# Performance work log

Hardware: AMD Instinct MI355X
Metric: run time of the kernel (lower is better)

## Reference

```python
import jax, jax.numpy as jnp
import numpy as np

N_NODES = 100000
N_EDGES = 3200000
F_IN = 16
HID = 64
K = 4
N_LAYERS = 3
SLOPE = 0.01  # LeakyReLU default negative slope


def _gcn_norm(src, dst, edge_weight, n):
    # PyG gcn_norm with add_self_loops=False: deg over targets
    deg = jax.ops.segment_sum(edge_weight, dst, num_segments=n)
    dinv = jnp.where(deg > 0, jax.lax.rsqrt(jnp.maximum(deg, 1e-30)), 0.0)
    return dinv[src] * edge_weight * dinv[dst]


def _tag_conv(x, src, dst, norm, Ws, b):
    # out = sum_{k=0..K} (A_norm^k x) @ Ws[k] + b ; Ws: [K+1, in, out]
    out = x @ Ws[0]
    h = x
    for k in range(1, Ws.shape[0]):
        msg = norm[:, None] * h[src]                      # [E, in]
        h = jax.ops.segment_sum(msg, dst, num_segments=x.shape[0])
        out = out + h @ Ws[k]
    return out + b


def leaky_relu(x):
    return jnp.where(x >= 0, x, SLOPE * x)


def setup_inputs() -> dict:
    key = jax.random.key(0)
    ks = jax.random.split(key, 10)
    x = jax.random.normal(ks[0], (N_NODES, F_IN), dtype=jnp.float32)
    edge_index = jax.random.randint(ks[1], (2, N_EDGES), 0, N_NODES, dtype=jnp.int64)
    edge_weight = jax.random.uniform(ks[2], (N_EDGES,), dtype=jnp.float32)
    batch = jnp.zeros((N_NODES,), dtype=jnp.int64)
    s1 = 1.0 / np.sqrt(F_IN)
    s2 = 1.0 / np.sqrt(HID)
    W1 = jax.random.uniform(ks[3], (K + 1, F_IN, HID), jnp.float32, -s1, s1)
    b1 = jnp.zeros((HID,), jnp.float32)
    W2 = jax.random.uniform(ks[4], (N_LAYERS - 1, K + 1, HID, HID), jnp.float32, -s2, s2)
    b2 = jnp.zeros((N_LAYERS - 1, HID), jnp.float32)
    Wout = jax.random.uniform(ks[5], (HID, 1), jnp.float32, -s2, s2)
    bout = jnp.zeros((1,), jnp.float32)
    return {"x": x, "edge_index": edge_index, "edge_weight": edge_weight,
            "batch": batch, "W1": W1, "b1": b1, "W2": W2, "b2": b2,
            "Wout": Wout, "bout": bout}


def reference(x, edge_index, edge_weight, batch, W1, b1, W2, b2, Wout, bout):
    src, dst = edge_index[0], edge_index[1]
    norm = _gcn_norm(src, dst, edge_weight, x.shape[0])
    h = _tag_conv(x, src, dst, norm, W1, b1)
    h = leaky_relu(h)  # dropout p=0 -> identity (inference)
    for i in range(N_LAYERS - 1):
        h = _tag_conv(h, src, dst, norm, W2[i], b2[i])
        h = leaky_relu(h)
    # reghead_layers == 1 -> singleLinear
    return h @ Wout + bout
```

## Files before the change

### kernel.cpp

```cpp
#include <hip/hip_runtime.h>


typedef unsigned long long u64;
typedef unsigned int u32;

__device__ __forceinline__ float h2f(unsigned short u) {
  _Float16 h;
  __builtin_memcpy(&h, &u, 2);
  return (float)h;
}
__device__ __forceinline__ unsigned short f2h(float f) {
  _Float16 h = (_Float16)f;
  unsigned short u;
  __builtin_memcpy(&u, &h, 2);
  return u;
}
__device__ __forceinline__ ushort4 pack_h(float4 v) {
  ushort4 r;
  r.x = f2h(v.x); r.y = f2h(v.y); r.z = f2h(v.z); r.w = f2h(v.w);
  return r;
}
__device__ __forceinline__ float4 unpack_h(ushort4 u) {
  return make_float4(h2f(u.x), h2f(u.y), h2f(u.z), h2f(u.w));
}

__device__ __forceinline__ void fmix_lo(float& acc, u32 wsh, u32 h) {
  asm("v_fma_mix_f32 %0, %1, %2, %0 op_sel:[1,0,0] op_sel_hi:[1,1,0]"
      : "+v"(acc) : "v"(wsh), "v"(h));
}
__device__ __forceinline__ void fmix_hi(float& acc, u32 wsh, u32 h) {
  asm("v_fma_mix_f32 %0, %1, %2, %0 op_sel:[1,1,0] op_sel_hi:[1,1,0]"
      : "+v"(acc) : "v"(wsh), "v"(h));
}


__global__ __launch_bounds__(256) void k_hist(const int* __restrict__ dst, u32* __restrict__ H,
                                              int E, int CH, int NB,
                                              const float4* __restrict__ x4,
                                              ushort4* __restrict__ xh, int n4) {
  __shared__ u32 hc[1024];
  int tid = threadIdx.x, blk = blockIdx.x, nblk = gridDim.x;
  for (int i = tid; i < 1024; i += 256) hc[i] = 0;
  for (int i = blk * 256 + tid; i < n4; i += nblk * 256) xh[i] = pack_h(x4[i]);
  __syncthreads();
  int e0 = blk * CH, e1 = min(E, e0 + CH);
  for (int e = e0 + tid; e < e1; e += 256) atomicAdd(&hc[((u32)dst[e]) >> 7], 1u);
  __syncthreads();
  for (int c = tid; c < NB; c += 256) H[(size_t)c * nblk + blk] = hc[c];
}

__global__ void scanH_blocks(u32* __restrict__ H, u32* __restrict__ bsum, int n) {
  __shared__ u32 s[256];
  int tid = threadIdx.x;
  int i = blockIdx.x * 256 + tid;
  u32 v = (i < n) ? H[i] : 0;
  s[tid] = v;
  __syncthreads();
#pragma unroll
  for (int off = 1; off < 256; off <<= 1) {
    u32 t = (tid >= off) ? s[tid - off] : 0;
    __syncthreads();
    s[tid] += t;
    __syncthreads();
  }
  if (i < n) H[i] = s[tid] - v;
  if (tid == 255) bsum[blockIdx.x] = s[255];
}

__global__ void scanH_sums(u32* __restrict__ bsum, int nb) {
  __shared__ u32 s[1024];
  __shared__ u32 carry;
  int tid = threadIdx.x;
  if (tid == 0) carry = 0;
  __syncthreads();
  for (int base = 0; base < nb; base += 1024) {
    int i = base + tid;
    u32 v = (i < nb) ? bsum[i] : 0;
    s[tid] = v;
    __syncthreads();
#pragma unroll
    for (int off = 1; off < 1024; off <<= 1) {
      u32 t = (tid >= off) ? s[tid - off] : 0;
      __syncthreads();
      s[tid] += t;
      __syncthreads();
    }
    u32 c = carry;
    if (i < nb) bsum[i] = s[tid] - v + c;
    __syncthreads();
    if (tid == 1023) carry = c + s[1023];
    __syncthreads();
  }
}

__global__ void scanH_add(u32* __restrict__ H, const u32* __restrict__ bsum, int n) {
  int i = blockIdx.x * blockDim.x + threadIdx.x;
  if (i < n) H[i] += bsum[i >> 8];
}

__global__ __launch_bounds__(256) void k_scatter(const int* __restrict__ src,
                                                 const int* __restrict__ dst,
                                                 const float* __restrict__ w,
                                                 const u32* __restrict__ H,
                                                 u64* __restrict__ sorted, int E, int CH, int NB) {
  __shared__ u32 cur[1024];
  int tid = threadIdx.x, blk = blockIdx.x, nblk = gridDim.x;
  for (int c = tid; c < NB; c += 256) cur[c] = H[(size_t)c * nblk + blk];
  __syncthreads();
  int e0 = blk * CH, e1 = min(E, e0 + CH);
  for (int e = e0 + tid; e < e1; e += 256) {
    int d = dst[e];
    int c = ((u32)d) >> 7;
    u32 p = atomicAdd(&cur[c], 1u);
    u64 it = (u64)(u32)src[e] | ((u64)((u32)d & 127u) << 17) |
             ((u64)__float_as_uint(w[e]) << 24);
    sorted[p] = it;
  }
}

#define BCAP 6144
__global__ __launch_bounds__(256) void k_bucket(u64* __restrict__ sorted,
                                                const u32* __restrict__ H, int NBLK,
                                                int* __restrict__ ptr, float* __restrict__ dinv,
                                                int N, int E, int NB) {
  __shared__ u64 stage[BCAP];
  __shared__ u32 cnt[128], base[128], cur[128], tmp[128];
  __shared__ float ws[128];
  int c = blockIdx.x, tid = threadIdx.x;
  int b0 = (int)H[(size_t)c * NBLK];
  int b1 = (c + 1 < NB) ? (int)H[(size_t)(c + 1) * NBLK] : E;
  int m = b1 - b0;
  if (tid < 128) { cnt[tid] = 0; ws[tid] = 0.f; }
  __syncthreads();
  for (int i = tid; i < m; i += 256) {
    u64 it = sorted[b0 + i];
    stage[i] = it;
    int lo = (int)((it >> 17) & 127u);
    atomicAdd(&cnt[lo], 1u);
    atomicAdd(&ws[lo], __uint_as_float((u32)(it >> 24)));
  }
  __syncthreads();
  u32 v = (tid < 128) ? cnt[tid] : 0;
  if (tid < 128) tmp[tid] = v;
  __syncthreads();
#pragma unroll
  for (int off = 1; off < 128; off <<= 1) {
    u32 t = 0;
    if (tid < 128 && tid >= off) t = tmp[tid - off];
    __syncthreads();
    if (tid < 128) tmp[tid] += t;
    __syncthreads();
  }
  if (tid < 128) {
    base[tid] = tmp[tid] - v;
    cur[tid] = tmp[tid] - v;
    int node = c * 128 + tid;
    if (node < N) {
      ptr[node] = b0 + (int)base[tid];
      float d = ws[tid];
      dinv[node] = (d > 0.f) ? rsqrtf(fmaxf(d, 1e-30f)) : 0.f;
    }
  }
  if (c == NB - 1 && tid == 0) ptr[N] = E;
  __syncthreads();
  for (int i = tid; i < m; i += 256) {
    u64 it = stage[i];
    int lo = (int)((it >> 17) & 127u);
    u32 p = atomicAdd(&cur[lo], 1u);
    sorted[b0 + (int)p] = it;
  }
}

__global__ __launch_bounds__(256) void k_pack(const u64* __restrict__ sorted,
                                              const float* __restrict__ dinv,
                                              const u32* __restrict__ H, int NBLK,
                                              u32* __restrict__ ep, int E, int NB) {
  int c = blockIdx.x;
  int b0 = (int)H[(size_t)c * NBLK];
  int b1 = (c + 1 < NB) ? (int)H[(size_t)(c + 1) * NBLK] : E;
  for (int i = b0 + threadIdx.x; i < b1; i += 256) {
    u64 it = sorted[i];
    int s = (int)(it & 0x1FFFFu);
    int dn = c * 128 + (int)((it >> 17) & 127u);
    float wv = __uint_as_float((u32)(it >> 24));
    float nv = dinv[s] * wv * dinv[dn];
    ep[i] = ((u32)f2h(nv) << 17) | (u32)s;
  }
}

__device__ __forceinline__ void acc_e2(float4& a, u32 pe, uint2 hh) {
  u32 wsh = pe >> 1;
  fmix_lo(a.x, wsh, hh.x); fmix_hi(a.y, wsh, hh.x);
  fmix_lo(a.z, wsh, hh.y); fmix_hi(a.w, wsh, hh.y);
}

template <int F4>
__device__ __forceinline__ float4 gather(const int* __restrict__ ptr, const u32* __restrict__ ep,
                                         const ushort4* __restrict__ hin, int node, int f4) {
  int e0 = ptr[node], e1 = ptr[node + 1];
  float4 a = make_float4(0.f, 0.f, 0.f, 0.f);
  int e = e0;
  while (e < e1 && (e & 3)) {
    u32 pe = ep[e];
    acc_e2(a, pe, *(const uint2*)(hin + ((u32)(pe & 0x1FFFFu) * F4 + f4)));
    ++e;
  }
  int nq = (e1 - e) >> 2;
  if (nq > 0) {
    uint4 p = *(const uint4*)(ep + e);
    uint2 h0 = *(const uint2*)(hin + ((u32)(p.x & 0x1FFFFu) * F4 + f4));
    uint2 h1 = *(const uint2*)(hin + ((u32)(p.y & 0x1FFFFu) * F4 + f4));
    uint2 h2 = *(const uint2*)(hin + ((u32)(p.z & 0x1FFFFu) * F4 + f4));
    uint2 h3 = *(const uint2*)(hin + ((u32)(p.w & 0x1FFFFu) * F4 + f4));
    for (int q = 1; q < nq; ++q) {
      uint4 pn = *(const uint4*)(ep + e + 4 * q);
      uint2 g0 = *(const uint2*)(hin + ((u32)(pn.x & 0x1FFFFu) * F4 + f4));
      uint2 g1 = *(const uint2*)(hin + ((u32)(pn.y & 0x1FFFFu) * F4 + f4));
      uint2 g2 = *(const uint2*)(hin + ((u32)(pn.z & 0x1FFFFu) * F4 + f4));
      uint2 g3 = *(const uint2*)(hin + ((u32)(pn.w & 0x1FFFFu) * F4 + f4));
      acc_e2(a, p.x, h0); acc_e2(a, p.y, h1);
      acc_e2(a, p.z, h2); acc_e2(a, p.w, h3);
      p = pn; h0 = g0; h1 = g1; h2 = g2; h3 = g3;
    }
    acc_e2(a, p.x, h0); acc_e2(a, p.y, h1);
    acc_e2(a, p.z, h2); acc_e2(a, p.w, h3);
    e += nq * 4;
  }
  while (e < e1) {
    u32 pe = ep[e];
    acc_e2(a, pe, *(const uint2*)(hin + ((u32)(pe & 0x1FFFFu) * F4 + f4)));
    ++e;
  }
  return a;
}

__device__ __forceinline__ void acc8(float4& a0, float4& a1, u32 pe, uint4 r) {
  u32 wsh = pe >> 1;
  fmix_lo(a0.x, wsh, r.x); fmix_hi(a0.y, wsh, r.x);
  fmix_lo(a0.z, wsh, r.y); fmix_hi(a0.w, wsh, r.y);
  fmix_lo(a1.x, wsh, r.z); fmix_hi(a1.y, wsh, r.z);
  fmix_lo(a1.z, wsh, r.w); fmix_hi(a1.w, wsh, r.w);
}

__device__ __forceinline__ uint4 row16(const ushort4* __restrict__ hin, u32 pe, u32 foff) {
  return *(const uint4*)(hin + ((u32)(pe & 0x1FFFFu) * 16u + foff));
}

__device__ __forceinline__ void gather64o(const int* __restrict__ ptr, const u32* __restrict__ ep,
                                          const ushort4* __restrict__ hin, int node,
                                          int f8, int o, float4& a0, float4& a1) {
  int e0 = ptr[node], e1 = ptr[node + 1];
  const u32 foff = 2u * (u32)f8;
  int e = e0;
  while (e < e1 && (e & 3)) {
    if ((e & 1) == o) {
      u32 pe = ep[e];
      acc8(a0, a1, pe, row16(hin, pe, foff));
    }
    ++e;
  }
  int nq = (e1 - e) >> 2;
  int m = (nq > o) ? ((nq - o + 1) >> 1) : 0;
  const u32* qb = ep + e + 4 * o;
  if (m > 0) {
    uint4 pA = *(const uint4*)(qb);
    uint4 A0 = row16(hin, pA.x, foff), A1 = row16(hin, pA.y, foff);
    uint4 A2 = row16(hin, pA.z, foff), A3 = row16(hin, pA.w, foff);
    int j = 0;
    while (j + 2 < m) {
      uint4 pB = *(const uint4*)(qb + 8 * (j + 1));
      uint4 B0 = row16(hin, pB.x, foff), B1 = row16(hin, pB.y, foff);
      uint4 B2 = row16(hin, pB.z, foff), B3 = row16(hin, pB.w, foff);
      acc8(a0, a1, pA.x, A0); acc8(a0, a1, pA.y, A1);
      acc8(a0, a1, pA.z, A2); acc8(a0, a1, pA.w, A3);
      pA = *(const uint4*)(qb + 8 * (j + 2));
      A0 = row16(hin, pA.x, foff); A1 = row16(hin, pA.y, foff);
      A2 = row16(hin, pA.z, foff); A3 = row16(hin, pA.w, foff);
      acc8(a0, a1, pB.x, B0); acc8(a0, a1, pB.y, B1);
      acc8(a0, a1, pB.z, B2); acc8(a0, a1, pB.w, B3);
      j += 2;
    }
    if (j + 1 < m) {
      uint4 pB = *(const uint4*)(qb + 8 * (j + 1));
      uint4 B0 = row16(hin, pB.x, foff), B1 = row16(hin, pB.y, foff);
      uint4 B2 = row16(hin, pB.z, foff), B3 = row16(hin, pB.w, foff);
      acc8(a0, a1, pA.x, A0); acc8(a0, a1, pA.y, A1);
      acc8(a0, a1, pA.z, A2); acc8(a0, a1, pA.w, A3);
      acc8(a0, a1, pB.x, B0); acc8(a0, a1, pB.y, B1);
      acc8(a0, a1, pB.z, B2); acc8(a0, a1, pB.w, B3);
    } else {
      acc8(a0, a1, pA.x, A0); acc8(a0, a1, pA.y, A1);
      acc8(a0, a1, pA.z, A2); acc8(a0, a1, pA.w, A3);
    }
  }
  e += nq * 4;
  while (e < e1) {
    if ((e & 1) == o) {
      u32 pe = ep[e];
      acc8(a0, a1, pe, row16(hin, pe, foff));
    }
    ++e;
  }
}

__device__ __forceinline__ void mm_acc(const float* __restrict__ tl, const float4* __restrict__ Wl,
                                       int ln, int j4, float4& a) {
#pragma unroll 8
  for (int i = 0; i < 64; ++i) {
    float tv = tl[ln * 64 + ((((i >> 2) ^ ln) << 2) | (i & 3))];
    float4 wv = Wl[i * 16 + j4];
    a.x = fmaf(tv, wv.x, a.x); a.y = fmaf(tv, wv.y, a.y);
    a.z = fmaf(tv, wv.z, a.z); a.w = fmaf(tv, wv.w, a.w);
  }
}

template <bool FIRST, bool LAST, bool HEAD>
__launch_bounds__(256, 8)
__global__ void ptag64_k(const int* __restrict__ ptr, const u32* __restrict__ ep,
                         const ushort4* __restrict__ hin, ushort4* __restrict__ hout,
                         const float4* __restrict__ Wk4, const float4* __restrict__ W04,
                         ushort4* __restrict__ acch, const float4* __restrict__ bias4,
                         const float* __restrict__ Wout, const float* __restrict__ bout,
                         float* __restrict__ outv, int n) {
  __shared__ float4 Wl[1024];
  __shared__ float4 tl4[256];
  const float* tl = (const float*)tl4;
  int tid = threadIdx.x;
  for (int i = tid; i < 1024; i += 256) Wl[i] = Wk4[i];
  int gid = blockIdx.x * 256 + tid;
  int node = gid >> 4, j4 = gid & 15, ln = tid >> 4;
  const int o = j4 >> 3, f8 = j4 & 7;

  float4 a0 = make_float4(0.f, 0.f, 0.f, 0.f);
  float4 a1 = make_float4(0.f, 0.f, 0.f, 0.f);
  if (node < n) gather64o(ptr, ep, hin, node, f8, o, a0, a1);
  a0.x += __shfl_xor(a0.x, 8, 16); a0.y += __shfl_xor(a0.y, 8, 16);
  a0.z += __shfl_xor(a0.z, 8, 16); a0.w += __shfl_xor(a0.w, 8, 16);
  a1.x += __shfl_xor(a1.x, 8, 16); a1.y += __shfl_xor(a1.y, 8, 16);
  a1.z += __shfl_xor(a1.z, 8, 16); a1.w += __shfl_xor(a1.w, 8, 16);
  float4 t = (o == 0) ? a0 : a1;
  int g = 2 * f8 + o;
  if (node < n && !LAST) hout[(size_t)node * 16 + g] = pack_h(t);
  tl4[ln * 16 + (g ^ ln)] = t;
  __syncthreads();

  float4 a = make_float4(0.f, 0.f, 0.f, 0.f);
  if (!FIRST && node < n) a = unpack_h(acch[(size_t)node * 16 + j4]);
  mm_acc(tl, Wl, ln, j4, a);
  if (FIRST) {
    __syncthreads();
    for (int i = tid; i < 1024; i += 256) Wl[i] = W04[i];
    float4 own = make_float4(0.f, 0.f, 0.f, 0.f);
    if (node < n) own = unpack_h(hin[(size_t)node * 16 + j4]);
    tl4[ln * 16 + (j4 ^ ln)] = own;
    __syncthreads();
    mm_acc(tl, Wl, ln, j4, a);
  }
  if (node >= n) return;

  if (LAST) {
    float4 b = bias4[j4];
    a.x += b.x; a.y += b.y; a.z += b.z; a.w += b.w;
    a.x = (a.x >= 0.f) ? a.x : 0.01f * a.x;
    a.y = (a.y >= 0.f) ? a.y : 0.01f * a.y;
    a.z = (a.z >= 0.f) ? a.z : 0.01f * a.z;
    a.w = (a.w >= 0.f) ? a.w : 0.01f * a.w;
    if (HEAD) {
      float v = a.x * Wout[4 * j4] + a.y * Wout[4 * j4 + 1] +
                a.z * Wout[4 * j4 + 2] + a.w * Wout[4 * j4 + 3];
      v += __shfl_down(v, 8, 16);
      v += __shfl_down(v, 4, 16);
      v += __shfl_down(v, 2, 16);
      v += __shfl_down(v, 1, 16);
      if (j4 == 0) outv[node] = v + bout[0];
    } else {
      hout[(size_t)node * 16 + j4] = pack_h(a);
    }
  } else {
    acch[(size_t)node * 16 + j4] = pack_h(a);
  }
}

template <bool FIRST, bool LAST>
__launch_bounds__(256)
__global__ void ptag16_k(const int* __restrict__ ptr, const u32* __restrict__ ep,
                         const ushort4* __restrict__ hin, ushort4* __restrict__ hout,
                         const float4* __restrict__ Wk4, const float4* __restrict__ W04,
                         ushort4* __restrict__ acch, const float4* __restrict__ bias4,
                         ushort4* __restrict__ outbuf, int n) {
  __shared__ float4 Wl[256];
  __shared__ float4 W0l[FIRST ? 256 : 1];
  __shared__ float4 tl4[64 * 5];
  const float* tl = (const float*)tl4;
  int tid = threadIdx.x;
  Wl[tid] = Wk4[tid];
  if (FIRST) W0l[tid] = W04[tid];
  int gid = blockIdx.x * 256 + tid;
  int node = gid >> 2, q = tid & 3, ln = tid >> 2;

  float4 t = make_float4(0.f, 0.f, 0.f, 0.f);
  if (node < n) {
    t = gather<4>(ptr, ep, hin, node, q);
    if (!LAST) hout[(size_t)node * 4 + q] = pack_h(t);
  }
  tl4[ln * 5 + q] = t;
  __syncthreads();

  float4 a[4];
#pragma unroll
  for (int c = 0; c < 4; ++c) a[c] = make_float4(0.f, 0.f, 0.f, 0.f);
  if (!FIRST && node < n) {
#pragma unroll
    for (int c = 0; c < 4; ++c) a[c] = unpack_h(acch[(size_t)node * 16 + 4 * q + c]);
  }
#pragma unroll 4
  for (int i = 0; i < 16; ++i) {
    float tv = tl[ln * 20 + i];
#pragma unroll
    for (int c = 0; c < 4; ++c) {
      float4 wv = Wl[i * 16 + 4 * q + c];
      a[c].x = fmaf(tv, wv.x, a[c].x); a[c].y = fmaf(tv, wv.y, a[c].y);
      a[c].z = fmaf(tv, wv.z, a[c].z); a[c].w = fmaf(tv, wv.w, a[c].w);
    }
  }
  if (FIRST) {
    __syncthreads();
    float4 own = make_float4(0.f, 0.f, 0.f, 0.f);
    if (node < n) own = unpack_h(hin[(size_t)node * 4 + q]);
    tl4[ln * 5 + q] = own;
    __syncthreads();
#pragma unroll 4
    for (int i = 0; i < 16; ++i) {
      float tv = tl[ln * 20 + i];
#pragma unroll
      for (int c = 0; c < 4; ++c) {
        float4 wv = W0l[i * 16 + 4 * q + c];
        a[c].x = fmaf(tv, wv.x, a[c].x); a[c].y = fmaf(tv, wv.y, a[c].y);
        a[c].z = fmaf(tv, wv.z, a[c].z); a[c].w = fmaf(tv, wv.w, a[c].w);
      }
    }
  }
  if (node >= n) return;

  if (LAST) {
#pragma unroll
    for (int c = 0; c < 4; ++c) {
      float4 b = bias4[4 * q + c];
      a[c].x += b.x; a[c].y += b.y; a[c].z += b.z; a[c].w += b.w;
      a[c].x = (a[c].x >= 0.f) ? a[c].x : 0.01f * a[c].x;
      a[c].y = (a[c].y >= 0.f) ? a[c].y : 0.01f * a[c].y;
      a[c].z = (a[c].z >= 0.f) ? a[c].z : 0.01f * a[c].z;
      a[c].w = (a[c].w >= 0.f) ? a[c].w : 0.01f * a[c].w;
      outbuf[(size_t)node * 16 + 4 * q + c] = pack_h(a[c]);
    }
  } else {
#pragma unroll
    for (int c = 0; c < 4; ++c) acch[(size_t)node * 16 + 4 * q + c] = pack_h(a[c]);
  }
}

extern "C" void kernel_launch(void* const* d_in, const int* in_sizes, int n_in,
                              void* d_out, int out_size, void* d_ws, size_t ws_size,
                              hipStream_t stream) {
  const float* x    = (const float*)d_in[0];
  const int*   ei   = (const int*)d_in[1];
  const float* ew   = (const float*)d_in[2];
  const float* W1   = (const float*)d_in[4];
  const float* b1   = (const float*)d_in[5];
  const float* W2   = (const float*)d_in[6];
  const float* b2   = (const float*)d_in[7];
  const float* Wout = (const float*)d_in[8];
  const float* bout = (const float*)d_in[9];
  float* out = (float*)d_out;

  const int N = in_sizes[0] / 16;
  const int E = in_sizes[2];
  const int* src = ei;
  const int* dst = ei + E;

  const int NBH = 1024;
  const int CH = (E + NBH - 1) / NBH;
  const int NB = (N + 127) >> 7;
  const int HN = NB * NBH;

  char* ws = (char*)d_ws;
  size_t off = 0;
  auto alloc = [&](size_t bytes) {
    char* p = ws + off;
    off = (off + bytes + 255) & ~(size_t)255;
    return p;
  };
  u32*     H      = (u32*)alloc((size_t)HN * 4);
  u32*     bsum   = (u32*)alloc(16384);
  float*   dinv   = (float*)alloc((size_t)N * 4);
  int*     ptr    = (int*)alloc(((size_t)N + 1) * 4);
  u64*     sorted = (u64*)alloc((size_t)E * 8);
  u32*     ep     = (u32*)alloc((size_t)E * 4);
  ushort4* xh     = (ushort4*)alloc((size_t)N * 16 * 2);
  ushort4* hb0    = (ushort4*)alloc((size_t)N * 64 * 2);
  ushort4* hb1    = (ushort4*)alloc((size_t)N * 64 * 2);
  ushort4* hb2    = (ushort4*)alloc((size_t)N * 64 * 2);
  ushort4* acch   = (ushort4*)alloc((size_t)N * 64 * 2);

  k_hist<<<NBH, 256, 0, stream>>>(dst, H, E, CH, NB, (const float4*)x, xh, N * 4);
  scanH_blocks<<<HN / 256, 256, 0, stream>>>(H, bsum, HN);
  scanH_sums<<<1, 1024, 0, stream>>>(bsum, HN / 256);
  scanH_add<<<HN / 256, 256, 0, stream>>>(H, bsum, HN);
  k_scatter<<<NBH, 256, 0, stream>>>(src, dst, ew, H, sorted, E, CH, NB);
  k_bucket<<<NB, 256, 0, stream>>>(sorted, H, NBH, ptr, dinv, N, E, NB);
  k_pack<<<NB, 256, 0, stream>>>(sorted, dinv, H, NBH, ep, E, NB);

  int g4  = (N * 4 + 255) / 256;
  int g16 = (N * 16 + 255) / 256;

  auto W1k = [&](int k) { return (const float4*)(W1 + (size_t)k * 1024); };
  auto W2k = [&](int l, int k) { return (const float4*)(W2 + ((size_t)l * 5 + k) * 4096); };

  ptag16_k<true,  false><<<g4, 256, 0, stream>>>(ptr, ep, xh,  hb0, W1k(1), W1k(0), acch, nullptr, nullptr, N);
  ptag16_k<false, false><<<g4, 256, 0, stream>>>(ptr, ep, hb0, hb1, W1k(2), nullptr, acch, nullptr, nullptr, N);
  ptag16_k<false, false><<<g4, 256, 0, stream>>>(ptr, ep, hb1, hb0, W1k(3), nullptr, acch, nullptr, nullptr, N);
  ptag16_k<false, true ><<<g4, 256, 0, stream>>>(ptr, ep, hb0, nullptr, W1k(4), nullptr, acch,
                                                 (const float4*)b1, hb2, N);

  ptag64_k<true,  false, false><<<g16, 256, 0, stream>>>(ptr, ep, hb2, hb0, W2k(0,1), W2k(0,0), acch,
                                                         nullptr, nullptr, nullptr, nullptr, N);
  ptag64_k<false, false, false><<<g16, 256, 0, stream>>>(ptr, ep, hb0, hb1, W2k(0,2), nullptr, acch,
                                                         nullptr, nullptr, nullptr, nullptr, N);
  ptag64_k<false, false, false><<<g16, 256, 0, stream>>>(ptr, ep, hb1, hb0, W2k(0,3), nullptr, acch,
                                                         nullptr, nullptr, nullptr, nullptr, N);
  ptag64_k<false, true,  false><<<g16, 256, 0, stream>>>(ptr, ep, hb0, hb2, W2k(0,4), nullptr, acch,
                                                         (const float4*)b2, nullptr, nullptr, nullptr, N);
  ptag64_k<true,  false, false><<<g16, 256, 0, stream>>>(ptr, ep, hb2, hb0, W2k(1,1), W2k(1,0), acch,
                                                         nullptr, nullptr, nullptr, nullptr, N);
  ptag64_k<false, false, false><<<g16, 256, 0, stream>>>(ptr, ep, hb0, hb1, W2k(1,2), nullptr, acch,
                                                         nullptr, nullptr, nullptr, nullptr, N);
  ptag64_k<false, false, false><<<g16, 256, 0, stream>>>(ptr, ep, hb1, hb0, W2k(1,3), nullptr, acch,
                                                         nullptr, nullptr, nullptr, nullptr, N);
  ptag64_k<false, true,  true ><<<g16, 256, 0, stream>>>(ptr, ep, hb0, nullptr, W2k(1,4), nullptr, acch,
                                                         (const float4*)(b2 + 64), Wout, bout, out, N);
}
```

Before: 922.0 us.

## Locally sort edges per block in LDS before coalesced scatter to buckets

The scatter kernel now processes two histogram chunks per block. It builds a local bucket histogram and prefix scan in shared memory, then computes a local permutation of edge indices. Writes to the global sorted array then go out in bucket-contiguous runs, giving more coalesced stores than random per-edge scattered writes. The cost is an extra pass over dst, more shared memory (which can lower occupancy), and reliance on the chunk fitting SIDX_CAP and on the H offsets of consecutive blocks being contiguous per bucket.

```diff
diff --git a/kernel.cpp b/kernel.cpp
--- a/kernel.cpp
+++ b/kernel.cpp
@@ -98,23 +98,55 @@
   if (i < n) H[i] += bsum[i >> 8];
 }
 
-__global__ __launch_bounds__(256) void k_scatter(const int* __restrict__ src,
-                                                 const int* __restrict__ dst,
-                                                 const float* __restrict__ w,
-                                                 const u32* __restrict__ H,
-                                                 u64* __restrict__ sorted, int E, int CH, int NB) {
-  __shared__ u32 cur[1024];
-  int tid = threadIdx.x, blk = blockIdx.x, nblk = gridDim.x;
-  for (int c = tid; c < NB; c += 256) cur[c] = H[(size_t)c * nblk + blk];
-  __syncthreads();
-  int e0 = blk * CH, e1 = min(E, e0 + CH);
+#define SIDX_CAP 6400
+__global__ __launch_bounds__(256) void k_scatter2(const int* __restrict__ src,
+                                                  const int* __restrict__ dst,
+                                                  const float* __restrict__ w,
+                                                  const u32* __restrict__ H,
+                                                  u64* __restrict__ sorted,
+                                                  int E, int CH, int NB, int NBHIST) {
+  __shared__ u32 cnt[1024], base[1024], cur[1024], Hb[1024];
+  __shared__ u32 tmp[256];
+  __shared__ unsigned short sidx[SIDX_CAP];
+  int tid = threadIdx.x, blk = blockIdx.x;
+  int e0 = blk * 2 * CH, e1 = min(E, e0 + 2 * CH);
+  int m = e1 - e0;
+  for (int c = tid; c < 1024; c += 256) cnt[c] = 0;
+  __syncthreads();
+  for (int e = e0 + tid; e < e1; e += 256)
+    atomicAdd(&cnt[((u32)dst[e]) >> 7], 1u);
+  __syncthreads();
+  u32 c0 = cnt[4 * tid], c1 = cnt[4 * tid + 1], c2 = cnt[4 * tid + 2], c3 = cnt[4 * tid + 3];
+  u32 s = c0 + c1 + c2 + c3;
+  tmp[tid] = s;
+  __syncthreads();
+#pragma unroll
+  for (int off = 1; off < 256; off <<= 1) {
+    u32 t = (tid >= off) ? tmp[tid - off] : 0;
+    __syncthreads();
+    tmp[tid] += t;
+    __syncthreads();
+  }
+  u32 pre = tmp[tid] - s;
+  base[4 * tid] = pre;           cur[4 * tid] = pre;
+  base[4 * tid + 1] = pre + c0;  cur[4 * tid + 1] = pre + c0;
+  base[4 * tid + 2] = pre + c0 + c1;       cur[4 * tid + 2] = pre + c0 + c1;
+  base[4 * tid + 3] = pre + c0 + c1 + c2;  cur[4 * tid + 3] = pre + c0 + c1 + c2;
+  for (int c = tid; c < NB; c += 256) Hb[c] = H[(size_t)c * NBHIST + 2 * blk];
+  __syncthreads();
   for (int e = e0 + tid; e < e1; e += 256) {
-    int d = dst[e];
-    int c = ((u32)d) >> 7;
-    u32 p = atomicAdd(&cur[c], 1u);
-    u64 it = (u64)(u32)src[e] | ((u64)((u32)d & 127u) << 17) |
-             ((u64)__float_as_uint(w[e]) << 24);
-    sorted[p] = it;
+    u32 c = ((u32)dst[e]) >> 7;
+    u32 r = atomicAdd(&cur[c], 1u);
+    sidx[r] = (unsigned short)(e - e0);
+  }
+  __syncthreads();
+  for (int r = tid; r < m; r += 256) {
+    int i = e0 + (int)sidx[r];
+    int d = dst[i];
+    u32 c = ((u32)d) >> 7;
+    u64 it = (u64)(u32)src[i] | ((u64)((u32)d & 127u) << 17) |
+             ((u64)__float_as_uint(w[i]) << 24);
+    sorted[Hb[c] + (r - base[c])] = it;
   }
 }
 
@@ -480,6 +512,7 @@
 
   const int NBH = 1024;
   const int CH = (E + NBH - 1) / NBH;
+  const int NSC = NBH / 2;
   const int NB = (N + 127) >> 7;
   const int HN = NB * NBH;
 
@@ -506,7 +539,7 @@
   scanH_blocks<<<HN / 256, 256, 0, stream>>>(H, bsum, HN);
   scanH_sums<<<1, 1024, 0, stream>>>(bsum, HN / 256);
   scanH_add<<<HN / 256, 256, 0, stream>>>(H, bsum, HN);
-  k_scatter<<<NBH, 256, 0, stream>>>(src, dst, ew, H, sorted, E, CH, NB);
+  k_scatter2<<<NSC, 256, 0, stream>>>(src, dst, ew, H, sorted, E, CH, NB, NBH);
   k_bucket<<<NB, 256, 0, stream>>>(sorted, H, NBH, ptr, dinv, N, E, NB);
   k_pack<<<NB, 256, 0, stream>>>(sorted, dinv, H, NBH, ep, E, NB);
 
```

Measured after the change: 932.8 us. No clear change (+1.2%).
